# Performance work log

Measured on AMD Instinct MI355X. Metric: run time of the kernel, lower is better.

Reference implementation:

```python
import jax, jax.numpy as jnp
import numpy as np
import math

N = 6000      # nodes
E = 96000     # edges
HID = 32      # hidden_dim
DEPTH = 3
RATIO = 0.2
BN_EPS = 1e-5


def _gcn(x, A, W, b):
    # GCNConv(improved=True): A_hat = A + 2I, out = D^-1/2 A_hat D^-1/2 (x W) + b
    # A[i, j] = weight of edge j -> i (message-passing orientation)
    n = A.shape[0]
    idx = jnp.arange(n)
    Ah = A.at[idx, idx].add(2.0)
    deg = Ah.sum(axis=1)
    dinv = jnp.where(deg > 0, jax.lax.rsqrt(deg), 0.0)
    An = dinv[:, None] * Ah * dinv[None, :]
    return An @ (x @ W) + b


def _two_hop(A):
    # GraphUNet.augment_adj: add self loops, sparse A@A, remove self loops
    n = A.shape[0]
    idx = jnp.arange(n)
    A1 = A.at[idx, idx].add(1.0)
    A2 = A1 @ A1
    return A2.at[idx, idx].set(0.0)


def _unpack(fl):
    x = fl[0]
    wd = list(fl[1:9:2]); bd = list(fl[2:9:2])
    pv = list(fl[9:12])
    wu = list(fl[12:18:2]); bu = list(fl[13:18:2])
    return x, (wd, bd, pv, wu, bu, fl[18], fl[19])


def _forward(x, edge_index, params):
    wd, bd, pv, wu, bu, bn_g, bn_b = params
    n = x.shape[0]
    # dense adjacency, transposed so A[dst, src] = edge weight
    A = jnp.zeros((n, n), x.dtype).at[edge_index[1], edge_index[0]].add(1.0)
    h = jax.nn.relu(_gcn(x, A, wd[0], bd[0]))
    xs, As, perms = [h], [A], []
    Acur = A
    for i in range(DEPTH):
        A2 = _two_hop(Acur)
        # TopKPooling: score = tanh(x.p / ||p||), keep top ceil(ratio*n)
        p = pv[i]
        score = jnp.tanh((h @ p) / jnp.linalg.norm(p))
        k = math.ceil(RATIO * h.shape[0])
        vals, perm = jax.lax.top_k(score, k)
        h = h[perm] * vals[:, None]
        Acur = A2[perm][:, perm]
        h = jax.nn.relu(_gcn(h, Acur, wd[i + 1], bd[i + 1]))
        if i < DEPTH - 1:
            xs.append(h)
            As.append(Acur)
        perms.append(perm)
    for i in range(DEPTH):
        j = DEPTH - 1 - i
        up = jnp.zeros_like(xs[j]).at[perms[j]].set(h)  # unpool
        h = _gcn(xs[j] + up, As[j], wu[i], bu[i])       # sum_res=True
        if i < DEPTH - 1:
            h = jax.nn.relu(h)
    # PFNet5 tail: BatchNorm1d(1) (batch stats) + sigmoid on channel 0
    v = h[:, 0]
    mean = v.mean()
    var = jnp.mean((v - mean) ** 2)
    r1 = jax.nn.sigmoid(bn_g[0] * (v - mean) * jax.lax.rsqrt(var + BN_EPS) + bn_b[0])
    return h.at[:, 0].set(r1)


def setup_inputs() -> dict:
    key = jax.random.key(0)
    ks = jax.random.split(key, 20)
    def nrm(k, shape, s=0.1):
        return jax.random.normal(k, shape, jnp.float32) * s
    inp = {
        "x": jax.random.normal(ks[0], (N, 3), jnp.float32),
        "edge_index": jax.random.randint(ks[1], (2, E), 0, N),
    }
    dims_down = [(3, HID), (HID, HID), (HID, HID), (HID, HID)]
    for i, (di, do) in enumerate(dims_down):
        inp[f"w_down{i}"] = nrm(ks[2 + i], (di, do))
        inp[f"b_down{i}"] = jnp.zeros((do,), jnp.float32)
    for i in range(3):
        inp[f"pool{i}"] = nrm(ks[6 + i], (HID,))
    dims_up = [(HID, HID), (HID, HID), (HID, 4)]
    for i, (di, do) in enumerate(dims_up):
        inp[f"w_up{i}"] = nrm(ks[9 + i], (di, do))
        inp[f"b_up{i}"] = jnp.zeros((do,), jnp.float32)
    inp["bn_gamma"] = jnp.ones((1,), jnp.float32)
    inp["bn_beta"] = jnp.zeros((1,), jnp.float32)
    return inp


def reference(x, edge_index, w_down0, b_down0, w_down1, b_down1, w_down2, b_down2,
              w_down3, b_down3, pool0, pool1, pool2, w_up0, b_up0, w_up1, b_up1,
              w_up2, b_up2, bn_gamma, bn_beta):
    fl = (x, w_down0, b_down0, w_down1, b_down1, w_down2, b_down2, w_down3, b_down3,
          pool0, pool1, pool2, w_up0, b_up0, w_up1, b_up1, w_up2, b_up2,
          bn_gamma, bn_beta)
    x_, params = _unpack(fl)
    return _forward(x_, edge_index, params)
```

## Files before the change

kernel.cpp:

```cpp
#include <hip/hip_runtime.h>
#include <hip/hip_bf16.h>

#define TPB 256

__device__ __forceinline__ float block_sum_f(float v, float* fs){
  int tid = threadIdx.x, lane = tid & 63, w = tid >> 6;
  #pragma unroll
  for(int o = 32; o > 0; o >>= 1) v += __shfl_down(v, o, 64);
  __syncthreads();
  if(lane == 0) fs[w] = v;
  __syncthreads();
  return fs[0] + fs[1] + fs[2] + fs[3];
}

__global__ void k_count(const int* __restrict__ ei, int E, int* __restrict__ cnt){
  int e = blockIdx.x*blockDim.x + threadIdx.x;
  if(e < E) atomicAdd(&cnt[ei[E + e]], 1);
}

template<int IPT>
__global__ void k_scan(const int* __restrict__ cnt, int n, int* __restrict__ rowptr){
  int tid = threadIdx.x;
  int base = tid * IPT;
  int loc[IPT]; int s = 0;
  #pragma unroll
  for(int q = 0; q < IPT; ++q){ int i = base + q; int v = (i < n) ? cnt[i] : 0; s += v; loc[q] = s; }
  int lane = tid & 63, w = tid >> 6;
  int ss = s;
  #pragma unroll
  for(int o = 1; o < 64; o <<= 1){ int t = __shfl_up(ss, o, 64); if(lane >= o) ss += t; }
  __shared__ int wsum[16];
  if(lane == 63) wsum[w] = ss;
  __syncthreads();
  if(tid < 16){
    int t = wsum[tid];
    for(int o = 1; o < 16; o <<= 1){ int uu = __shfl_up(t, o, 64); if(tid >= o) t += uu; }
    wsum[tid] = t;
  }
  __syncthreads();
  int excl = ss - s + (w > 0 ? wsum[w-1] : 0);
  if(tid == 0) rowptr[0] = 0;
  #pragma unroll
  for(int q = 0; q < IPT; ++q){ int i = base + q; if(i < n) rowptr[i+1] = excl + loc[q]; }
}

__global__ void k_fill(const int* __restrict__ ei, int E, const int* __restrict__ rowptr,
                       int* __restrict__ fill, int* __restrict__ colidx){
  int e = blockIdx.x*blockDim.x + threadIdx.x;
  if(e >= E) return;
  int d = ei[E + e], s = ei[e];
  int p = rowptr[d] + atomicAdd(&fill[d], 1);
  colidx[p] = s;
}

__global__ void k_agg3(const float* __restrict__ x, const int* __restrict__ cnt,
                       const int* __restrict__ rowptr, const int* __restrict__ colidx,
                       float* __restrict__ dinv0, float* __restrict__ xa, int n){
  int i = blockIdx.x*blockDim.x + threadIdx.x;
  if(i >= n) return;
  float di = rsqrtf((float)cnt[i] + 2.0f);
  dinv0[i] = di;
  float s0 = 2.f*di*x[i*3], s1 = 2.f*di*x[i*3+1], s2 = 2.f*di*x[i*3+2];
  for(int q = rowptr[i]; q < rowptr[i+1]; ++q){
    int j = colidx[q];
    float dj = rsqrtf((float)cnt[j] + 2.0f);
    s0 += dj*x[j*3]; s1 += dj*x[j*3+1]; s2 += dj*x[j*3+2];
  }
  xa[i*3] = s0; xa[i*3+1] = s1; xa[i*3+2] = s2;
}

__global__ void k_gcn0(const float* __restrict__ xa, const float* __restrict__ W0,
                       const float* __restrict__ b0, const float* __restrict__ dinv0,
                       const float* __restrict__ p0, float* __restrict__ h0,
                       float* __restrict__ score, int n){
  int t = blockIdx.x*blockDim.x + threadIdx.x;
  if(t >= n*32) return;
  int i = t >> 5, c = t & 31;
  float y = dinv0[i]*(xa[i*3]*W0[c] + xa[i*3+1]*W0[32+c] + xa[i*3+2]*W0[64+c]) + b0[c];
  y = fmaxf(y, 0.f);
  h0[t] = y;
  float pv = p0[c]; float sd = y*pv, nn = pv*pv;
  #pragma unroll
  for(int o = 16; o > 0; o >>= 1){ sd += __shfl_xor(sd, o, 32); nn += __shfl_xor(nn, o, 32); }
  if(c == 0) score[i] = tanhf(sd / sqrtf(nn));
}

template<int NMAX>
__global__ __launch_bounds__(1024)
void k_pool(const float* __restrict__ score, int n, int k,
            int* __restrict__ perm, int* __restrict__ rank){
  __shared__ unsigned keys[NMAX];
  __shared__ int bins[2048];
  __shared__ int wsum[16];
  __shared__ unsigned s_prefix;
  __shared__ int s_rk, s_found, s_cntgt;
  int tid = threadIdx.x, lane = tid & 63, w = tid >> 6;
  for(int i = tid; i < n; i += 1024){
    rank[i] = -1;
    unsigned uu = __float_as_uint(score[i]);
    uu ^= (uu & 0x80000000u) ? 0xFFFFFFFFu : 0x80000000u;
    keys[i] = uu;
  }
  if(tid == 0){ s_prefix = 0u; s_rk = k; }
  __syncthreads();
  for(int pass = 0; pass < 3; ++pass){
    const int width = (pass < 2) ? 11 : 10;
    const int shift = (pass == 0) ? 21 : ((pass == 1) ? 10 : 0);
    const int nb = 1 << width;
    for(int b2 = tid; b2 < nb; b2 += 1024) bins[b2] = 0;
    __syncthreads();
    unsigned prefix = s_prefix;
    int rk = s_rk;
    const int hs = shift + width;
    for(int i = tid; i < n; i += 1024){
      unsigned kk = keys[i];
      bool match = (pass == 0) || ((kk >> hs) == (prefix >> hs));
      if(match) atomicAdd(&bins[(kk >> shift) & (nb-1)], 1);
    }
    __syncthreads();
    int ipt = (nb + 1023) >> 10;
    int loc0 = 0, loc1 = 0, s = 0;
    { int r = tid*ipt; int v = (r < nb) ? bins[nb-1-r] : 0; s += v; loc0 = s;
      if(ipt == 2){ int r2 = r+1; int v2 = (r2 < nb) ? bins[nb-1-r2] : 0; s += v2; loc1 = s; } }
    int ss = s;
    #pragma unroll
    for(int o = 1; o < 64; o <<= 1){ int t2 = __shfl_up(ss, o, 64); if(lane >= o) ss += t2; }
    if(lane == 63) wsum[w] = ss;
    __syncthreads();
    if(tid < 16){
      int t2 = wsum[tid];
      #pragma unroll
      for(int o = 1; o < 16; o <<= 1){ int u2 = __shfl_up(t2, o, 64); if(tid >= o) t2 += u2; }
      wsum[tid] = t2;
    }
    __syncthreads();
    int excl = ss - s + (w ? wsum[w-1] : 0);
    { int r = tid*ipt; if(r < nb) bins[nb-1-r] = excl + loc0;
      if(ipt == 2){ int r2 = r+1; if(r2 < nb) bins[nb-1-r2] = excl + loc1; } }
    __syncthreads();
    for(int b2 = tid; b2 < nb; b2 += 1024){
      int cge = bins[b2];
      int cgt = (b2+1 < nb) ? bins[b2+1] : 0;
      if(cge >= rk && cgt < rk){ s_found = b2; s_cntgt = cgt; }
    }
    __syncthreads();
    if(tid == 0){ s_prefix |= ((unsigned)s_found) << shift; s_rk -= s_cntgt; }
    __syncthreads();
  }
  unsigned T = s_prefix;
  int r = s_rk;
  int cgt_total = k - r;
  int CH = (n + 1023) >> 10;
  int base = tid*CH, c_gt = 0, c_eq = 0;
  for(int q = 0; q < CH; ++q){
    int i = base+q;
    if(i < n){ unsigned uu = keys[i]; c_gt += (uu > T); c_eq += (uu == T); }
  }
  int packed = c_gt*8192 + c_eq;
  int ss2 = packed;
  #pragma unroll
  for(int o = 1; o < 64; o <<= 1){ int t2 = __shfl_up(ss2, o, 64); if(lane >= o) ss2 += t2; }
  if(lane == 63) wsum[w] = ss2;
  __syncthreads();
  if(tid < 16){
    int t2 = wsum[tid];
    #pragma unroll
    for(int o = 1; o < 16; o <<= 1){ int u2 = __shfl_up(t2, o, 64); if(tid >= o) t2 += u2; }
    wsum[tid] = t2;
  }
  __syncthreads();
  int excl2 = ss2 - packed + (w ? wsum[w-1] : 0);
  int gt_before = excl2 / 8192, eq_before = excl2 % 8192;
  for(int q = 0; q < CH; ++q){
    int i = base+q;
    if(i >= n) continue;
    unsigned uu = keys[i];
    if(uu > T){ int pos = gt_before++; perm[pos] = i; rank[i] = pos; }
    else if(uu == T){
      int tr = eq_before++;
      if(tr < r){ int pos = cgt_total + tr; perm[pos] = i; rank[i] = pos; }
    }
  }
}

__global__ void k_gather_mm(const float* __restrict__ h, const float* __restrict__ score,
                            const int* __restrict__ perm, const float* __restrict__ W,
                            float* __restrict__ hw, int k){
  int t = blockIdx.x*blockDim.x + threadIdx.x;
  if(t >= k*32) return;
  int i = t >> 5, c = t & 31;
  int idx = perm[i];
  float sc = score[idx];
  const float* hr = h + (size_t)idx*32;
  float s = 0.f;
  #pragma unroll
  for(int d = 0; d < 32; ++d) s += hr[d]*W[d*32 + c];
  hw[t] = sc*s;
}

__global__ __launch_bounds__(256)
void k_build_B1(const int* __restrict__ rowptr, const int* __restrict__ colidx,
                const int* __restrict__ perm1, const int* __restrict__ rank1, int K1,
                float* __restrict__ dinv1, int* __restrict__ rowbeg, int* __restrict__ rowend,
                int* __restrict__ col1, float* __restrict__ val1, int* __restrict__ cursor){
  __shared__ float row[1216];
  __shared__ int wsum[4];
  __shared__ float fs[4];
  __shared__ int s_base;
  int tid = threadIdx.x, lane = tid & 63, w = tid >> 6;
  int i = blockIdx.x;
  for(int j = tid; j < K1; j += 256) row[j] = 0.f;
  __syncthreads();
  int d = perm1[i];
  int b = rowptr[d], len = rowptr[d+1]-b;
  for(int p = tid; p < len; p += 256){
    int s = colidx[b+p]; int rs = rank1[s];
    if(rs >= 0) atomicAdd(&row[rs], 2.0f);
  }
  for(int ww = tid; ww < len*8; ww += 256){
    int p = ww >> 3, sub = ww & 7;
    int s = colidx[b+p];
    for(int q = rowptr[s]+sub, qe = rowptr[s+1]; q < qe; q += 8){
      int r2 = rank1[colidx[q]];
      if(r2 >= 0) atomicAdd(&row[r2], 1.0f);
    }
  }
  __syncthreads();
  if(tid == 0) row[i] = 0.f;
  __syncthreads();
  float s = 0.f;
  for(int j = tid; j < K1; j += 256) s += row[j];
  float tot = block_sum_f(s, fs);
  if(tid == 0){ dinv1[i] = rsqrtf(tot + 2.0f); row[i] = 1.0f; }
  __syncthreads();
  int CH = (K1 + 255) >> 8;
  int base = tid*CH, cnt = 0;
  for(int q = 0; q < CH; ++q){ int j = base+q; if(j < K1 && row[j] != 0.f) ++cnt; }
  int ss = cnt;
  #pragma unroll
  for(int o = 1; o < 64; o <<= 1){ int t2 = __shfl_up(ss, o, 64); if(lane >= o) ss += t2; }
  if(lane == 63) wsum[w] = ss;
  __syncthreads();
  if(tid < 4){
    int t2 = wsum[tid];
    for(int o = 1; o < 4; o <<= 1){ int u2 = __shfl_up(t2, o, 64); if(tid >= o) t2 += u2; }
    wsum[tid] = t2;
  }
  __syncthreads();
  if(tid == 0) s_base = atomicAdd(cursor, wsum[3]);
  __syncthreads();
  int off = s_base + ss - cnt + (w ? wsum[w-1] : 0);
  for(int q = 0; q < CH; ++q){
    int j = base+q;
    if(j < K1 && row[j] != 0.f){ col1[off] = j; val1[off] = row[j]; ++off; }
  }
  if(tid == 0){ rowbeg[i] = s_base; rowend[i] = s_base + wsum[3]; }
}

template<bool RELU, bool SCORE>
__global__ void k_spmm(const int* __restrict__ rb, const int* __restrict__ re,
                       const int* __restrict__ ci, const float* __restrict__ cv,
                       const float* __restrict__ hw, const float* __restrict__ dinv,
                       const float* __restrict__ bias, float* __restrict__ out, int n,
                       const float* __restrict__ pvec, float* __restrict__ score){
  int t = blockIdx.x*blockDim.x + threadIdx.x;
  if(t >= n*32) return;
  int i = t >> 5, c = t & 31;
  float acc = dinv[i]*hw[t];
  for(int p = rb[i], e = re[i]; p < e; ++p){
    int j = ci[p];
    acc += cv[p]*dinv[j]*hw[j*32 + c];
  }
  float y = dinv[i]*acc + bias[c];
  y = RELU ? fmaxf(y, 0.f) : y;
  out[t] = y;
  if(SCORE){
    float pv = pvec[c];
    float sd = y*pv, nn = pv*pv;
    #pragma unroll
    for(int o = 16; o > 0; o >>= 1){ sd += __shfl_xor(sd, o, 32); nn += __shfl_xor(nn, o, 32); }
    if(c == 0) score[i] = tanhf(sd / sqrtf(nn));
  }
}

__global__ __launch_bounds__(256)
void k_twohop_sp(const int* __restrict__ rb, const int* __restrict__ re,
                 const int* __restrict__ ci, const float* __restrict__ cv,
                 const int* __restrict__ perm2, const int* __restrict__ rank2,
                 float* __restrict__ C2, float* __restrict__ dinv2, int K2){
  __shared__ float acc[256];
  __shared__ float fs[4];
  int i = blockIdx.x, tid = threadIdx.x;
  for(int j = tid; j < K2; j += 256) acc[j] = 0.f;
  __syncthreads();
  int qi = perm2[i];
  int b = rb[qi], len = re[qi]-b;
  for(int ww = tid; ww < len*8; ww += 256){
    int p = b + (ww >> 3), sub = ww & 7;
    int t = ci[p]; float v = cv[p];
    for(int q = rb[t] + sub, qe = re[t]; q < qe; q += 8){
      int j = rank2[ci[q]];
      if(j >= 0) atomicAdd(&acc[j], v*cv[q]);
    }
  }
  __syncthreads();
  if(tid == 0) acc[i] = 0.f;
  __syncthreads();
  float s = 0.f;
  for(int j = tid; j < K2; j += 256) s += acc[j];
  float tot = block_sum_f(s, fs);
  if(tid == 0) dinv2[i] = rsqrtf(tot + 2.0f);
  for(int j = tid; j < K2; j += 256) C2[(size_t)i*K2 + j] = acc[j];
}

template<bool RELU, bool SCORE>
__global__ __launch_bounds__(256)
void k_dgcn(const float* __restrict__ C, const float* __restrict__ hw,
            const float* __restrict__ dinv, const float* __restrict__ bias,
            float* __restrict__ out, int n, const float* __restrict__ pvec,
            float* __restrict__ score){
  __shared__ float sh[8][32];
  int i = blockIdx.x;
  int c = threadIdx.x & 31, sg = threadIdx.x >> 5;
  const float* row = C + (size_t)i*n;
  float a = 0.f;
  for(int t = sg; t < n; t += 8) a += row[t]*dinv[t]*hw[t*32 + c];
  sh[sg][c] = a;
  __syncthreads();
  if(sg == 0){
    float aa = sh[0][c]+sh[1][c]+sh[2][c]+sh[3][c]+sh[4][c]+sh[5][c]+sh[6][c]+sh[7][c];
    aa += 2.f*dinv[i]*hw[i*32 + c];
    float y = dinv[i]*aa + bias[c];
    y = RELU ? fmaxf(y, 0.f) : y;
    out[i*32 + c] = y;
    if(SCORE){
      float pv = pvec[c];
      float sd = y*pv, nn = pv*pv;
      #pragma unroll
      for(int o = 16; o > 0; o >>= 1){ sd += __shfl_xor(sd, o, 32); nn += __shfl_xor(nn, o, 32); }
      if(c == 0) score[i] = tanhf(sd / sqrtf(nn));
    }
  }
}

__global__ __launch_bounds__(256)
void k_twohop_d3(const float* __restrict__ C2, int n, const int* __restrict__ perm3,
                 int k, float* __restrict__ C3, float* __restrict__ dinv3){
  __shared__ float acc[4][64];
  int i = blockIdx.x, tid = threadIdx.x;
  int col = tid & 63, st = tid >> 6;
  int qi = perm3[i];
  int qj = (col < k) ? perm3[col] : 0;
  float a = 0.f;
  if(col < k){
    for(int tt = st; tt < n; tt += 4){
      float av = C2[(size_t)qi*n + tt] + ((tt == qi) ? 1.f : 0.f);
      float bv = C2[(size_t)tt*n + qj] + ((tt == qj) ? 1.f : 0.f);
      a += av * bv;
    }
  }
  acc[st][col] = a;
  __syncthreads();
  if(st == 0){
    float v = acc[0][col]+acc[1][col]+acc[2][col]+acc[3][col];
    if(col == i) v = 0.f;
    if(col < k) C3[(size_t)i*k + col] = v;
    float sv = (col < k) ? v : 0.f;
    #pragma unroll
    for(int o = 32; o > 0; o >>= 1) sv += __shfl_down(sv, o, 64);
    if(col == 0) dinv3[i] = rsqrtf(sv + 2.0f);
  }
}

template<int COUT, bool DINV>
__global__ void k_addup_mm(const float* __restrict__ base, const float* __restrict__ h,
                           const int* __restrict__ rank, const float* __restrict__ W,
                           const float* __restrict__ dinv, float* __restrict__ out, int n){
  int t = blockIdx.x*blockDim.x + threadIdx.x;
  if(t >= n*COUT) return;
  int i = t / COUT, c = t - i*COUT;
  int r = rank[i];
  const float* br = base + (size_t)i*32;
  const float* hr = h + (size_t)(r >= 0 ? r : 0)*32;
  float s = 0.f;
  #pragma unroll
  for(int d = 0; d < 32; ++d){
    float z = br[d] + ((r >= 0) ? hr[d] : 0.f);
    s += z * W[d*COUT + c];
  }
  out[t] = DINV ? (dinv[i]*s) : s;
}

__global__ void k_gcn_final(const int* __restrict__ rowptr, const int* __restrict__ colidx,
                            const float* __restrict__ hw4, const float* __restrict__ dinv0,
                            const float* __restrict__ bias, float* __restrict__ out, int n,
                            float* __restrict__ bnp, float* __restrict__ bnq){
  __shared__ float fs[4];
  int t = blockIdx.x*blockDim.x + threadIdx.x;
  float vs = 0.f, vq = 0.f;
  if(t < n*4){
    int i = t >> 2, c = t & 3;
    float acc = 2.f*hw4[t];
    for(int q = rowptr[i]; q < rowptr[i+1]; ++q) acc += hw4[colidx[q]*4 + c];
    float y = dinv0[i]*acc + bias[c];
    out[t] = y;
    if(c == 0){ vs = y; vq = y*y; }
  }
  float bs = block_sum_f(vs, fs);
  float bq = block_sum_f(vq, fs);
  if(threadIdx.x == 0){ bnp[blockIdx.x] = bs; bnq[blockIdx.x] = bq; }
}

__global__ void k_bn_finish(float* __restrict__ out, int n, int nblk,
                            const float* __restrict__ bnp, const float* __restrict__ bnq,
                            const float* __restrict__ g, const float* __restrict__ b){
  __shared__ float fs[4];
  int tid = threadIdx.x;
  float sv = (tid < nblk) ? bnp[tid] : 0.f;
  float qv = (tid < nblk) ? bnq[tid] : 0.f;
  float tsum = block_sum_f(sv, fs);
  float tsq  = block_sum_f(qv, fs);
  float mean = tsum / n;
  float var  = tsq / n - mean*mean;
  float scale = g[0]*rsqrtf(var + 1e-5f);
  float beta  = b[0];
  for(int i = blockIdx.x*blockDim.x + tid; i < n; i += gridDim.x*blockDim.x){
    float r = scale*(out[i*4] - mean) + beta;
    out[i*4] = 1.f/(1.f + expf(-r));
  }
}

extern "C" void kernel_launch(void* const* d_in, const int* in_sizes, int n_in,
                              void* d_out, int out_size, void* d_ws, size_t ws_size,
                              hipStream_t stream){
  const float* x  =(const float*)d_in[0];
  const int*   ei =(const int*)  d_in[1];
  const float* W0 =(const float*)d_in[2];  const float* b0 =(const float*)d_in[3];
  const float* W1 =(const float*)d_in[4];  const float* b1 =(const float*)d_in[5];
  const float* W2 =(const float*)d_in[6];  const float* b2 =(const float*)d_in[7];
  const float* W3 =(const float*)d_in[8];  const float* b3 =(const float*)d_in[9];
  const float* p0 =(const float*)d_in[10];
  const float* p1 =(const float*)d_in[11];
  const float* p2 =(const float*)d_in[12];
  const float* Wu0=(const float*)d_in[13]; const float* bu0=(const float*)d_in[14];
  const float* Wu1=(const float*)d_in[15]; const float* bu1=(const float*)d_in[16];
  const float* Wu2=(const float*)d_in[17]; const float* bu2=(const float*)d_in[18];
  const float* bng=(const float*)d_in[19]; const float* bnb=(const float*)d_in[20];
  float* out = (float*)d_out;

  const int n0 = in_sizes[0] / 3;
  const int E  = in_sizes[1] / 2;
  const int K1 = (n0 + 4) / 5;
  const int K2 = (K1 + 4) / 5;
  const int K3 = (K2 + 4) / 5;
  const int CAP1 = 512*1024;

  char* wsp = (char*)d_ws; size_t off = 0;
  auto alloc = [&](size_t bytes)->char*{
    char* p = wsp + off; off = (off + bytes + 255) & ~((size_t)255); return p;
  };

  int*   zreg   = (int*)  alloc((size_t)(2*n0+64)*4);
  int*   cnt    = zreg;
  int*   fillc  = zreg + n0;
  int*   cursor = zreg + 2*n0;
  int*   rowptr = (int*)  alloc((size_t)(n0+1)*4);
  int*   colidx = (int*)  alloc((size_t)E*4);
  float* dinv0  = (float*)alloc((size_t)n0*4);
  float* xa     = (float*)alloc((size_t)n0*3*4);
  float* h0     = (float*)alloc((size_t)n0*32*4);
  float* score  = (float*)alloc((size_t)n0*4);
  int*   perm1  = (int*)  alloc((size_t)K1*4);
  int*   rank1  = (int*)  alloc((size_t)n0*4);
  float* hw1    = (float*)alloc((size_t)K1*32*4);
  float* dinv1  = (float*)alloc((size_t)K1*4);
  int*   rowbeg1= (int*)  alloc((size_t)K1*4);
  int*   rowend1= (int*)  alloc((size_t)K1*4);
  int*   col1   = (int*)  alloc((size_t)CAP1*4);
  float* val1   = (float*)alloc((size_t)CAP1*4);
  float* h1     = (float*)alloc((size_t)K1*32*4);
  int*   perm2  = (int*)  alloc((size_t)K2*4);
  int*   rank2  = (int*)  alloc((size_t)K1*4);
  float* hw2    = (float*)alloc((size_t)K2*32*4);
  float* C2     = (float*)alloc((size_t)K2*K2*4);
  float* dinv2  = (float*)alloc((size_t)K2*4);
  float* h2     = (float*)alloc((size_t)K2*32*4);
  int*   perm3  = (int*)  alloc((size_t)K3*4);
  int*   rank3  = (int*)  alloc((size_t)K2*4);
  float* hw3    = (float*)alloc((size_t)K3*32*4);
  float* C3     = (float*)alloc((size_t)K3*K3*4);
  float* dinv3  = (float*)alloc((size_t)K3*4);
  float* h3     = (float*)alloc((size_t)K3*32*4);
  float* hu2    = (float*)alloc((size_t)K2*32*4);
  float* hu1    = (float*)alloc((size_t)K1*32*4);
  float* hw4    = (float*)alloc((size_t)n0*4*4);
  float* bnp    = (float*)alloc((size_t)128*4);
  float* bnq    = (float*)alloc((size_t)128*4);

  hipMemsetAsync(zreg, 0, (size_t)(2*n0+64)*4, stream);

  const int gE  = (E + TPB - 1) / TPB;
  const int gBN = (n0*4 + TPB - 1) / TPB;
  k_count  <<<gE, TPB, 0, stream>>>(ei, E, cnt);
  k_scan<6><<<1, 1024, 0, stream>>>(cnt, n0, rowptr);
  k_fill   <<<gE, TPB, 0, stream>>>(ei, E, rowptr, fillc, colidx);
  k_agg3<<<(n0+TPB-1)/TPB, TPB, 0, stream>>>(x, cnt, rowptr, colidx, dinv0, xa, n0);
  k_gcn0<<<(n0*32+TPB-1)/TPB, TPB, 0, stream>>>(xa, W0, b0, dinv0, p0, h0, score, n0);
  k_pool<6144><<<1, 1024, 0, stream>>>(score, n0, K1, perm1, rank1);
  k_gather_mm<<<(K1*32+TPB-1)/TPB, TPB, 0, stream>>>(h0, score, perm1, W1, hw1, K1);
  k_build_B1<<<K1, 256, 0, stream>>>(rowptr, colidx, perm1, rank1, K1,
                                     dinv1, rowbeg1, rowend1, col1, val1, cursor);
  k_spmm<true,true><<<(K1*32+TPB-1)/TPB, TPB, 0, stream>>>(rowbeg1, rowend1, col1, val1,
                                                           hw1, dinv1, b1, h1, K1, p1, score);
  k_pool<1216><<<1, 1024, 0, stream>>>(score, K1, K2, perm2, rank2);
  k_gather_mm<<<(K2*32+TPB-1)/TPB, TPB, 0, stream>>>(h1, score, perm2, W2, hw2, K2);
  k_twohop_sp<<<K2, 256, 0, stream>>>(rowbeg1, rowend1, col1, val1, perm2, rank2, C2, dinv2, K2);
  k_dgcn<true,true><<<K2, 256, 0, stream>>>(C2, hw2, dinv2, b2, h2, K2, p2, score);
  k_pool<256><<<1, 1024, 0, stream>>>(score, K2, K3, perm3, rank3);
  k_gather_mm<<<(K3*32+TPB-1)/TPB, TPB, 0, stream>>>(h2, score, perm3, W3, hw3, K3);
  k_twohop_d3<<<K3, 256, 0, stream>>>(C2, K2, perm3, K3, C3, dinv3);
  k_dgcn<true,false><<<K3, 256, 0, stream>>>(C3, hw3, dinv3, b3, h3, K3, nullptr, nullptr);
  k_addup_mm<32,false><<<(K2*32+TPB-1)/TPB, TPB, 0, stream>>>(h2, h3, rank3, Wu0, nullptr, hw2, K2);
  k_dgcn<true,false><<<K2, 256, 0, stream>>>(C2, hw2, dinv2, bu0, hu2, K2, nullptr, nullptr);
  k_addup_mm<32,false><<<(K1*32+TPB-1)/TPB, TPB, 0, stream>>>(h1, hu2, rank2, Wu1, nullptr, hw1, K1);
  k_spmm<true,false><<<(K1*32+TPB-1)/TPB, TPB, 0, stream>>>(rowbeg1, rowend1, col1, val1,
                                                            hw1, dinv1, bu1, hu1, K1, nullptr, nullptr);
  k_addup_mm<4,true><<<(n0*4+TPB-1)/TPB, TPB, 0, stream>>>(h0, hu1, rank1, Wu2, dinv0, hw4, n0);
  k_gcn_final<<<gBN, TPB, 0, stream>>>(rowptr, colidx, hw4, dinv0, bu2, out, n0, bnp, bnq);
  k_bn_finish<<<24, TPB, 0, stream>>>(out, n0, gBN, bnp, bnq, bng, bnb);
}
```

Baseline: 214.2 us.

## Fuse first GCN aggregation, fold gather-matmul into pooling, prescale by dinv

Merges the 3-feature aggregation and first GCN layer into one per-node kernel. For levels 2 and 3 the gather-matmul is folded into the single-block top-k pooling kernel. The level-1 gather-matmul now runs after B1 is built, so its features can be pre-scaled by dinv, which drops the per-neighbour dinv load in the sparse aggregation. This removes several launches and some memory traffic. In exchange, the fused gather inside pooling runs on only one 1024-thread block, and the first layer has one thread per node writing 32 outputs with strided stores.

```diff
diff --git a/kernel.cpp b/kernel.cpp
--- a/kernel.cpp
+++ b/kernel.cpp
@@ -53,9 +53,11 @@
   colidx[p] = s;
 }
 
-__global__ void k_agg3(const float* __restrict__ x, const int* __restrict__ cnt,
+__global__ void k_gcn0(const float* __restrict__ x, const int* __restrict__ cnt,
                        const int* __restrict__ rowptr, const int* __restrict__ colidx,
-                       float* __restrict__ dinv0, float* __restrict__ xa, int n){
+                       const float* __restrict__ W0, const float* __restrict__ b0,
+                       const float* __restrict__ p0, float* __restrict__ dinv0,
+                       float* __restrict__ h0, float* __restrict__ score, int n){
   int i = blockIdx.x*blockDim.x + threadIdx.x;
   if(i >= n) return;
   float di = rsqrtf((float)cnt[i] + 2.0f);
@@ -66,29 +68,24 @@
     float dj = rsqrtf((float)cnt[j] + 2.0f);
     s0 += dj*x[j*3]; s1 += dj*x[j*3+1]; s2 += dj*x[j*3+2];
   }
-  xa[i*3] = s0; xa[i*3+1] = s1; xa[i*3+2] = s2;
-}
-
-__global__ void k_gcn0(const float* __restrict__ xa, const float* __restrict__ W0,
-                       const float* __restrict__ b0, const float* __restrict__ dinv0,
-                       const float* __restrict__ p0, float* __restrict__ h0,
-                       float* __restrict__ score, int n){
-  int t = blockIdx.x*blockDim.x + threadIdx.x;
-  if(t >= n*32) return;
-  int i = t >> 5, c = t & 31;
-  float y = dinv0[i]*(xa[i*3]*W0[c] + xa[i*3+1]*W0[32+c] + xa[i*3+2]*W0[64+c]) + b0[c];
-  y = fmaxf(y, 0.f);
-  h0[t] = y;
-  float pv = p0[c]; float sd = y*pv, nn = pv*pv;
-  #pragma unroll
-  for(int o = 16; o > 0; o >>= 1){ sd += __shfl_xor(sd, o, 32); nn += __shfl_xor(nn, o, 32); }
-  if(c == 0) score[i] = tanhf(sd / sqrtf(nn));
-}
-
-template<int NMAX>
+  float sd = 0.f, nn = 0.f;
+  #pragma unroll
+  for(int c = 0; c < 32; ++c){
+    float y = di*(s0*W0[c] + s1*W0[32+c] + s2*W0[64+c]) + b0[c];
+    y = fmaxf(y, 0.f);
+    h0[(size_t)i*32 + c] = y;
+    float pv = p0[c];
+    sd += y*pv; nn += pv*pv;
+  }
+  score[i] = tanhf(sd / sqrtf(nn));
+}
+
+template<int NMAX, bool GATHER>
 __global__ __launch_bounds__(1024)
 void k_pool(const float* __restrict__ score, int n, int k,
-            int* __restrict__ perm, int* __restrict__ rank){
+            int* __restrict__ perm, int* __restrict__ rank,
+            const float* __restrict__ h, const float* __restrict__ W,
+            float* __restrict__ hw){
   __shared__ unsigned keys[NMAX];
   __shared__ int bins[2048];
   __shared__ int wsum[16];
@@ -181,11 +178,24 @@
       if(tr < r){ int pos = cgt_total + tr; perm[pos] = i; rank[i] = pos; }
     }
   }
+  if(GATHER){
+    __syncthreads();
+    for(int t = tid; t < k*32; t += 1024){
+      int i = t >> 5, c = t & 31;
+      int idx = perm[i];
+      float sc = score[idx];
+      const float* hr = h + (size_t)idx*32;
+      float s = 0.f;
+      #pragma unroll
+      for(int d = 0; d < 32; ++d) s += hr[d]*W[d*32 + c];
+      hw[t] = sc*s;
+    }
+  }
 }
 
 __global__ void k_gather_mm(const float* __restrict__ h, const float* __restrict__ score,
                             const int* __restrict__ perm, const float* __restrict__ W,
-                            float* __restrict__ hw, int k){
+                            const float* __restrict__ dinv, float* __restrict__ hws, int k){
   int t = blockIdx.x*blockDim.x + threadIdx.x;
   if(t >= k*32) return;
   int i = t >> 5, c = t & 31;
@@ -195,7 +205,7 @@
   float s = 0.f;
   #pragma unroll
   for(int d = 0; d < 32; ++d) s += hr[d]*W[d*32 + c];
-  hw[t] = sc*s;
+  hws[t] = dinv[i]*(sc*s);
 }
 
 __global__ __launch_bounds__(256)
@@ -260,17 +270,14 @@
 template<bool RELU, bool SCORE>
 __global__ void k_spmm(const int* __restrict__ rb, const int* __restrict__ re,
                        const int* __restrict__ ci, const float* __restrict__ cv,
-                       const float* __restrict__ hw, const float* __restrict__ dinv,
+                       const float* __restrict__ hws, const float* __restrict__ dinv,
                        const float* __restrict__ bias, float* __restrict__ out, int n,
                        const float* __restrict__ pvec, float* __restrict__ score){
   int t = blockIdx.x*blockDim.x + threadIdx.x;
   if(t >= n*32) return;
   int i = t >> 5, c = t & 31;
-  float acc = dinv[i]*hw[t];
-  for(int p = rb[i], e = re[i]; p < e; ++p){
-    int j = ci[p];
-    acc += cv[p]*dinv[j]*hw[j*32 + c];
-  }
+  float acc = hws[t];
+  for(int p = rb[i], e = re[i]; p < e; ++p) acc += cv[p]*hws[ci[p]*32 + c];
   float y = dinv[i]*acc + bias[c];
   y = RELU ? fmaxf(y, 0.f) : y;
   out[t] = y;
@@ -467,7 +474,6 @@
   int*   rowptr = (int*)  alloc((size_t)(n0+1)*4);
   int*   colidx = (int*)  alloc((size_t)E*4);
   float* dinv0  = (float*)alloc((size_t)n0*4);
-  float* xa     = (float*)alloc((size_t)n0*3*4);
   float* h0     = (float*)alloc((size_t)n0*32*4);
   float* score  = (float*)alloc((size_t)n0*4);
   int*   perm1  = (int*)  alloc((size_t)K1*4);
@@ -504,25 +510,23 @@
   k_count  <<<gE, TPB, 0, stream>>>(ei, E, cnt);
   k_scan<6><<<1, 1024, 0, stream>>>(cnt, n0, rowptr);
   k_fill   <<<gE, TPB, 0, stream>>>(ei, E, rowptr, fillc, colidx);
-  k_agg3<<<(n0+TPB-1)/TPB, TPB, 0, stream>>>(x, cnt, rowptr, colidx, dinv0, xa, n0);
-  k_gcn0<<<(n0*32+TPB-1)/TPB, TPB, 0, stream>>>(xa, W0, b0, dinv0, p0, h0, score, n0);
-  k_pool<6144><<<1, 1024, 0, stream>>>(score, n0, K1, perm1, rank1);
-  k_gather_mm<<<(K1*32+TPB-1)/TPB, TPB, 0, stream>>>(h0, score, perm1, W1, hw1, K1);
+  k_gcn0<<<(n0+TPB-1)/TPB, TPB, 0, stream>>>(x, cnt, rowptr, colidx, W0, b0, p0,
+                                             dinv0, h0, score, n0);
+  k_pool<6144,false><<<1, 1024, 0, stream>>>(score, n0, K1, perm1, rank1, nullptr, nullptr, nullptr);
   k_build_B1<<<K1, 256, 0, stream>>>(rowptr, colidx, perm1, rank1, K1,
                                      dinv1, rowbeg1, rowend1, col1, val1, cursor);
+  k_gather_mm<<<(K1*32+TPB-1)/TPB, TPB, 0, stream>>>(h0, score, perm1, W1, dinv1, hw1, K1);
   k_spmm<true,true><<<(K1*32+TPB-1)/TPB, TPB, 0, stream>>>(rowbeg1, rowend1, col1, val1,
                                                            hw1, dinv1, b1, h1, K1, p1, score);
-  k_pool<1216><<<1, 1024, 0, stream>>>(score, K1, K2, perm2, rank2);
-  k_gather_mm<<<(K2*32+TPB-1)/TPB, TPB, 0, stream>>>(h1, score, perm2, W2, hw2, K2);
+  k_pool<1216,true><<<1, 1024, 0, stream>>>(score, K1, K2, perm2, rank2, h1, W2, hw2);
   k_twohop_sp<<<K2, 256, 0, stream>>>(rowbeg1, rowend1, col1, val1, perm2, rank2, C2, dinv2, K2);
   k_dgcn<true,true><<<K2, 256, 0, stream>>>(C2, hw2, dinv2, b2, h2, K2, p2, score);
-  k_pool<256><<<1, 1024, 0, stream>>>(score, K2, K3, perm3, rank3);
-  k_gather_mm<<<(K3*32+TPB-1)/TPB, TPB, 0, stream>>>(h2, score, perm3, W3, hw3, K3);
+  k_pool<256,true><<<1, 1024, 0, stream>>>(score, K2, K3, perm3, rank3, h2, W3, hw3);
   k_twohop_d3<<<K3, 256, 0, stream>>>(C2, K2, perm3, K3, C3, dinv3);
   k_dgcn<true,false><<<K3, 256, 0, stream>>>(C3, hw3, dinv3, b3, h3, K3, nullptr, nullptr);
   k_addup_mm<32,false><<<(K2*32+TPB-1)/TPB, TPB, 0, stream>>>(h2, h3, rank3, Wu0, nullptr, hw2, K2);
   k_dgcn<true,false><<<K2, 256, 0, stream>>>(C2, hw2, dinv2, bu0, hu2, K2, nullptr, nullptr);
-  k_addup_mm<32,false><<<(K1*32+TPB-1)/TPB, TPB, 0, stream>>>(h1, hu2, rank2, Wu1, nullptr, hw1, K1);
+  k_addup_mm<32,true><<<(K1*32+TPB-1)/TPB, TPB, 0, stream>>>(h1, hu2, rank2, Wu1, dinv1, hw1, K1);
   k_spmm<true,false><<<(K1*32+TPB-1)/TPB, TPB, 0, stream>>>(rowbeg1, rowend1, col1, val1,
                                                             hw1, dinv1, bu1, hu1, K1, nullptr, nullptr);
   k_addup_mm<4,true><<<(n0*4+TPB-1)/TPB, TPB, 0, stream>>>(h0, hu1, rank1, Wu2, dinv0, hw4, n0);
```

Result: slower. 222.8 us (+4.0%).
